# Optimization experiments

Measured on AMD Instinct MI355X. Metric: run time of the kernel, lower is better.

The kernel has to match this reference:

```python
import jax, jax.numpy as jnp
import numpy as np
import math

B, P = 4096, 512
WDT = 10          # lyr_wdt = number of irreps (multiplicity)
EPS2 = 1e-12      # NormActivation epsilon=1e-6, squared


def setup_inputs() -> dict:
    key = jax.random.key(0)
    ks = jax.random.split(key, 8)
    return {
        "invar_2b": jax.random.normal(ks[0], (B, P, 5), jnp.float32),
        "vectors_2b": jax.random.normal(ks[1], (B, P, 9), jnp.float32),
        # torch.nn.Linear params (stored as [in, out])
        "w1_0": jax.random.normal(ks[2], (5, WDT), jnp.float32) / math.sqrt(5.0),
        "b1_0": jnp.zeros((WDT,), jnp.float32),
        "w1_1": jax.random.normal(ks[3], (WDT, WDT), jnp.float32) / math.sqrt(float(WDT)),
        "b1_1": jnp.zeros((WDT,), jnp.float32),
        # o3.Linear weights (N(0,1) init, e3nn normalizes by sqrt(mul_in) in forward)
        "lin0_w": jax.random.normal(ks[4], (3, WDT), jnp.float32),
        "na0_b": jnp.zeros((WDT,), jnp.float32),   # NormActivation bias
        "lin1_w": jax.random.normal(ks[5], (WDT, WDT), jnp.float32),
        "na1_b": jnp.zeros((WDT,), jnp.float32),
        "final_w": jax.random.normal(ks[6], (WDT, 1), jnp.float32),
    }


def _self_intrc(x, w, bias):
    """o3.Linear (mul_in x 1o -> mul_out x 1o) + NormActivation(tanh, eps=1e-6, bias).

    x: [B, P, mul_in, 3]
    """
    mul_in = x.shape[-2]
    # single l=1 -> l=1 path; e3nn o3.Linear scales by 1/sqrt(fan_in)
    y = jnp.einsum('bpuc,uw->bpwc', x, w) / jnp.sqrt(jnp.float32(mul_in))
    # NormActivation: norm per irrep, clamped at eps^2 before sqrt
    n = jnp.sqrt(jnp.maximum(jnp.sum(y * y, axis=-1), EPS2))  # [B,P,mul_out]
    s = jnp.tanh(n + bias) / n                                # act(norm+b)/norm
    return y * s[..., None]


def reference(invar_2b, vectors_2b, w1_0, b1_0, w1_1, b1_1,
              lin0_w, na0_b, lin1_w, na1_b, final_w):
    # scalar branch: Linear(5,10) + ReLU, Linear(10,10) + ReLU
    y = jax.nn.relu(invar_2b @ w1_0 + b1_0)
    y = jax.nn.relu(y @ w1_1 + b1_1)              # [B, P, WDT] (10x0e)

    # equivariant branch: two self_intrc blocks on 3x1o -> 10x1o -> 10x1o
    v = vectors_2b.reshape(B, P, 3, 3)            # [B,P,3 irreps,3 comps]
    x = _self_intrc(v, lin0_w, na0_b)             # [B,P,WDT,3]
    x = _self_intrc(x, lin1_w, na1_b)             # [B,P,WDT,3]

    # ElementwiseTensorProduct(10x0e, 10x1o) -> 10x1o: per-irrep scalar gating
    x = y[..., None] * x                          # [B,P,WDT,3]

    # final o3.Linear 10x1o -> 1x1o
    x = jnp.einsum('bpuc,uw->bpwc', x, final_w) / jnp.sqrt(jnp.float32(WDT))
    return jnp.sum(x[..., 0, :], axis=1)          # sum over pairs -> [B, 3]
```

## Files before the change

### kernel.cpp

```cpp
#include <hip/hip_runtime.h>
#include <math.h>

#define BB 4096
#define PP 512
#define WDT 10
#define NP 4
#define NT 128

typedef float float2v __attribute__((ext_vector_type(2)));
typedef float float4v __attribute__((ext_vector_type(4)));

#define PKFMA(a, b, c) __builtin_elementwise_fma(a, b, c)
#define PKMAX(a, b)    __builtin_elementwise_max(a, b)
#define FENCE()        __builtin_amdgcn_sched_barrier(0)

__device__ __forceinline__ float2v bc2(float s) { return (float2v){s, s}; }

__device__ __forceinline__ float fast_tanh(float x) {
    float e = __builtin_amdgcn_exp2f(x * 2.8853900817779268f);
    return 1.0f - 2.0f * __builtin_amdgcn_rcpf(e + 1.0f);
}

__global__ __launch_bounds__(NT) void frc_2b_kernel(
    const float* __restrict__ invar,
    const float* __restrict__ vectors,
    const float* __restrict__ w1_0,
    const float* __restrict__ b1_0,
    const float* __restrict__ w1_1,
    const float* __restrict__ b1_1,
    const float* __restrict__ lin0_w,
    const float* __restrict__ na0_b,
    const float* __restrict__ lin1_w,
    const float* __restrict__ na1_b,
    const float* __restrict__ final_w,
    float* __restrict__ out)
{
    __shared__ float red[2][3];

    const int b   = blockIdx.x;
    const int tid = threadIdx.x;

    const float* iv0 = invar   + ((size_t)b * PP + tid * NP) * 5;
    const float* vv0 = vectors + ((size_t)b * PP + tid * NP) * 9;
    float in5a[NP][5];
    float v[NP][9];
    #pragma unroll
    for (int q = 0; q < 5; ++q) {
        float4v f = ((const float4v*)iv0)[q];
        #pragma unroll
        for (int r = 0; r < 4; ++r) {
            int idx = q * 4 + r;
            in5a[idx / 5][idx % 5] = f[r];
        }
    }
    #pragma unroll
    for (int q = 0; q < 9; ++q) {
        float4v f = ((const float4v*)vv0)[q];
        #pragma unroll
        for (int r = 0; r < 4; ++r) {
            int idx = q * 4 + r;
            v[idx / 9][idx % 9] = f[r];
        }
    }

    const float k3sq  = 0.33333333333333333f;
    const float k3k10 = 0.18257418583505536f;
    const float k10   = 0.31622776601683794f;
    const float2v z2  = {0.f, 0.f};

    float2v yp[NP][5];
    #pragma unroll
    for (int jp = 0; jp < 5; ++jp) {
        float2v bb = *(const float2v*)(b1_0 + 2 * jp);
        #pragma unroll
        for (int pr = 0; pr < NP; ++pr) yp[pr][jp] = bb;
    }
    #pragma unroll
    for (int i = 0; i < 5; ++i) {
        #pragma unroll
        for (int jp = 0; jp < 5; ++jp) {
            float2v wp = *(const float2v*)(w1_0 + i * WDT + 2 * jp);
            #pragma unroll
            for (int pr = 0; pr < NP; ++pr)
                yp[pr][jp] = PKFMA(wp, bc2(in5a[pr][i]), yp[pr][jp]);
        }
    }
    #pragma unroll
    for (int pr = 0; pr < NP; ++pr)
        #pragma unroll
        for (int jp = 0; jp < 5; ++jp) yp[pr][jp] = PKMAX(yp[pr][jp], z2);
    FENCE();

    float2v y2p[NP][5];
    #pragma unroll
    for (int jp = 0; jp < 5; ++jp) {
        float2v bb = *(const float2v*)(b1_1 + 2 * jp);
        #pragma unroll
        for (int pr = 0; pr < NP; ++pr) y2p[pr][jp] = bb;
    }
    #pragma unroll
    for (int k = 0; k < 5; ++k) {
        #pragma unroll
        for (int jp = 0; jp < 5; ++jp) {
            float2v wp = *(const float2v*)(w1_1 + k * WDT + 2 * jp);
            #pragma unroll
            for (int pr = 0; pr < NP; ++pr)
                y2p[pr][jp] = PKFMA(wp, bc2(yp[pr][k >> 1][k & 1]), y2p[pr][jp]);
        }
    }
    FENCE();
    #pragma unroll
    for (int k = 5; k < WDT; ++k) {
        #pragma unroll
        for (int jp = 0; jp < 5; ++jp) {
            float2v wp = *(const float2v*)(w1_1 + k * WDT + 2 * jp);
            #pragma unroll
            for (int pr = 0; pr < NP; ++pr)
                y2p[pr][jp] = PKFMA(wp, bc2(yp[pr][k >> 1][k & 1]), y2p[pr][jp]);
        }
    }
    #pragma unroll
    for (int pr = 0; pr < NP; ++pr)
        #pragma unroll
        for (int jp = 0; jp < 5; ++jp) y2p[pr][jp] = PKMAX(y2p[pr][jp], z2);
    FENCE();

    float2v c0p[NP][5], c1p[NP][5], c2p[NP][5];
    #pragma unroll
    for (int pr = 0; pr < NP; ++pr)
        #pragma unroll
        for (int jp = 0; jp < 5; ++jp) { c0p[pr][jp] = z2; c1p[pr][jp] = z2; c2p[pr][jp] = z2; }
    #pragma unroll
    for (int u = 0; u < 3; ++u) {
        #pragma unroll
        for (int jp = 0; jp < 5; ++jp) {
            float2v wp = *(const float2v*)(lin0_w + u * WDT + 2 * jp);
            #pragma unroll
            for (int pr = 0; pr < NP; ++pr) {
                c0p[pr][jp] = PKFMA(wp, bc2(v[pr][u * 3 + 0]), c0p[pr][jp]);
                c1p[pr][jp] = PKFMA(wp, bc2(v[pr][u * 3 + 1]), c1p[pr][jp]);
                c2p[pr][jp] = PKFMA(wp, bc2(v[pr][u * 3 + 2]), c2p[pr][jp]);
            }
        }
    }
    float2v x0p[NP][5], x1p[NP][5], x2p[NP][5];
    #pragma unroll
    for (int jp = 0; jp < 5; ++jp) {
        float2v nab = *(const float2v*)(na0_b + 2 * jp);
        #pragma unroll
        for (int pr = 0; pr < NP; ++pr) {
            float2v n2p = PKFMA(c0p[pr][jp], c0p[pr][jp],
                          PKFMA(c1p[pr][jp], c1p[pr][jp], c2p[pr][jp] * c2p[pr][jp]));
            float2v mp  = PKMAX(n2p * bc2(k3sq), bc2(1e-12f));
            float fh[2];
            #pragma unroll
            for (int h = 0; h < 2; ++h) {
                float m     = mp[h];
                float inv_n = __builtin_amdgcn_rsqf(m);
                float n     = m * inv_n;
                float t     = fast_tanh(n + nab[h]);
                fh[h] = t * inv_n * k3k10;
            }
            float2v fp = {fh[0], fh[1]};
            x0p[pr][jp] = c0p[pr][jp] * fp;
            x1p[pr][jp] = c1p[pr][jp] * fp;
            x2p[pr][jp] = c2p[pr][jp] * fp;
        }
    }
    FENCE();

    float2v e0p[NP][5], e1p[NP][5], e2p[NP][5];
    #pragma unroll
    for (int pr = 0; pr < NP; ++pr)
        #pragma unroll
        for (int jp = 0; jp < 5; ++jp) { e0p[pr][jp] = z2; e1p[pr][jp] = z2; e2p[pr][jp] = z2; }
    #pragma unroll
    for (int u = 0; u < 5; ++u) {
        #pragma unroll
        for (int jp = 0; jp < 5; ++jp) {
            float2v wp = *(const float2v*)(lin1_w + u * WDT + 2 * jp);
            #pragma unroll
            for (int pr = 0; pr < NP; ++pr) {
                e0p[pr][jp] = PKFMA(wp, bc2(x0p[pr][u >> 1][u & 1]), e0p[pr][jp]);
                e1p[pr][jp] = PKFMA(wp, bc2(x1p[pr][u >> 1][u & 1]), e1p[pr][jp]);
                e2p[pr][jp] = PKFMA(wp, bc2(x2p[pr][u >> 1][u & 1]), e2p[pr][jp]);
            }
        }
    }
    FENCE();
    #pragma unroll
    for (int u = 5; u < WDT; ++u) {
        #pragma unroll
        for (int jp = 0; jp < 5; ++jp) {
            float2v wp = *(const float2v*)(lin1_w + u * WDT + 2 * jp);
            #pragma unroll
            for (int pr = 0; pr < NP; ++pr) {
                e0p[pr][jp] = PKFMA(wp, bc2(x0p[pr][u >> 1][u & 1]), e0p[pr][jp]);
                e1p[pr][jp] = PKFMA(wp, bc2(x1p[pr][u >> 1][u & 1]), e1p[pr][jp]);
                e2p[pr][jp] = PKFMA(wp, bc2(x2p[pr][u >> 1][u & 1]), e2p[pr][jp]);
            }
        }
    }
    FENCE();

    float2v a0p = z2, a1p = z2, a2p = z2;
    #pragma unroll
    for (int jp = 0; jp < 5; ++jp) {
        float2v nab = *(const float2v*)(na1_b + 2 * jp);
        float2v fwp = *(const float2v*)(final_w + 2 * jp);
        #pragma unroll
        for (int pr = 0; pr < NP; ++pr) {
            float2v n2p = PKFMA(e0p[pr][jp], e0p[pr][jp],
                          PKFMA(e1p[pr][jp], e1p[pr][jp], e2p[pr][jp] * e2p[pr][jp]));
            float2v mp  = PKMAX(n2p, bc2(1e-12f));
            float gh[2];
            #pragma unroll
            for (int h = 0; h < 2; ++h) {
                float m     = mp[h];
                float inv_n = __builtin_amdgcn_rsqf(m);
                float n     = m * inv_n;
                float t     = fast_tanh(n + nab[h]);
                gh[h] = y2p[pr][jp][h] * t * inv_n * fwp[h];
            }
            float2v gp = {gh[0], gh[1]};
            a0p = PKFMA(e0p[pr][jp], gp, a0p);
            a1p = PKFMA(e1p[pr][jp], gp, a1p);
            a2p = PKFMA(e2p[pr][jp], gp, a2p);
        }
    }
    float acc0 = (a0p[0] + a0p[1]) * k10;
    float acc1 = (a1p[0] + a1p[1]) * k10;
    float acc2 = (a2p[0] + a2p[1]) * k10;

    #pragma unroll
    for (int off = 32; off > 0; off >>= 1) {
        acc0 += __shfl_down(acc0, off, 64);
        acc1 += __shfl_down(acc1, off, 64);
        acc2 += __shfl_down(acc2, off, 64);
    }
    const int wave = tid >> 6;
    if ((tid & 63) == 0) { red[wave][0] = acc0; red[wave][1] = acc1; red[wave][2] = acc2; }
    __syncthreads();
    if (tid == 0) {
        out[b * 3 + 0] = red[0][0] + red[1][0];
        out[b * 3 + 1] = red[0][1] + red[1][1];
        out[b * 3 + 2] = red[0][2] + red[1][2];
    }
}

extern "C" void kernel_launch(void* const* d_in, const int* in_sizes, int n_in,
                              void* d_out, int out_size, void* d_ws, size_t ws_size,
                              hipStream_t stream) {
    const float* invar   = (const float*)d_in[0];
    const float* vectors = (const float*)d_in[1];
    const float* w1_0    = (const float*)d_in[2];
    const float* b1_0    = (const float*)d_in[3];
    const float* w1_1    = (const float*)d_in[4];
    const float* b1_1    = (const float*)d_in[5];
    const float* lin0_w  = (const float*)d_in[6];
    const float* na0_b   = (const float*)d_in[7];
    const float* lin1_w  = (const float*)d_in[8];
    const float* na1_b   = (const float*)d_in[9];
    const float* final_w = (const float*)d_in[10];
    float* out = (float*)d_out;

    frc_2b_kernel<<<BB, NT, 0, stream>>>(invar, vectors, w1_0, b1_0, w1_1, b1_1,
                                         lin0_w, na0_b, lin1_w, na1_b, final_w, out);
}
```

Before: 184.5 us.

## Use 512-thread blocks covering two batch rows with two pairs per thread

Each thread now handles two pairs instead of four, and each block spans two batch rows with 512 threads, so the grid is halved. Loads switch from float4 to float2 vectors, and the reduction is reworked to sum four waves per row. The aim is more threads in flight to hide memory latency and fewer blocks to launch. The cost is less per-thread ILP and float2 loads that are less wide.

```diff
diff --git a/kernel.cpp b/kernel.cpp
--- a/kernel.cpp
+++ b/kernel.cpp
@@ -4,11 +4,10 @@
 #define BB 4096
 #define PP 512
 #define WDT 10
-#define NP 4
-#define NT 128
+#define NT 512
+#define NP 2
 
 typedef float float2v __attribute__((ext_vector_type(2)));
-typedef float float4v __attribute__((ext_vector_type(4)));
 
 #define PKFMA(a, b, c) __builtin_elementwise_fma(a, b, c)
 #define PKMAX(a, b)    __builtin_elementwise_max(a, b)
@@ -35,31 +34,31 @@
     const float* __restrict__ final_w,
     float* __restrict__ out)
 {
-    __shared__ float red[2][3];
-
-    const int b   = blockIdx.x;
+    __shared__ float red[8][3];
+
     const int tid = threadIdx.x;
-
-    const float* iv0 = invar   + ((size_t)b * PP + tid * NP) * 5;
-    const float* vv0 = vectors + ((size_t)b * PP + tid * NP) * 9;
+    const size_t g = (size_t)blockIdx.x * 1024 + (size_t)tid * 2;
+
+    const float* iv = invar   + g * 5;
+    const float* vv = vectors + g * 9;
+    float2v ivl[5], vvl[9];
+    #pragma unroll
+    for (int q = 0; q < 5; ++q) ivl[q] = ((const float2v*)iv)[q];
+    #pragma unroll
+    for (int q = 0; q < 9; ++q) vvl[q] = ((const float2v*)vv)[q];
     float in5a[NP][5];
     float v[NP][9];
     #pragma unroll
-    for (int q = 0; q < 5; ++q) {
-        float4v f = ((const float4v*)iv0)[q];
-        #pragma unroll
-        for (int r = 0; r < 4; ++r) {
-            int idx = q * 4 + r;
-            in5a[idx / 5][idx % 5] = f[r];
-        }
-    }
-    #pragma unroll
-    for (int q = 0; q < 9; ++q) {
-        float4v f = ((const float4v*)vv0)[q];
-        #pragma unroll
-        for (int r = 0; r < 4; ++r) {
-            int idx = q * 4 + r;
-            v[idx / 9][idx % 9] = f[r];
+    for (int pr = 0; pr < NP; ++pr) {
+        #pragma unroll
+        for (int i = 0; i < 5; ++i) {
+            int u = pr * 5 + i;
+            in5a[pr][i] = ivl[u >> 1][u & 1];
+        }
+        #pragma unroll
+        for (int i = 0; i < 9; ++i) {
+            int u = pr * 9 + i;
+            v[pr][i] = vvl[u >> 1][u & 1];
         }
     }
 
@@ -241,10 +240,20 @@
     const int wave = tid >> 6;
     if ((tid & 63) == 0) { red[wave][0] = acc0; red[wave][1] = acc1; red[wave][2] = acc2; }
     __syncthreads();
-    if (tid == 0) {
-        out[b * 3 + 0] = red[0][0] + red[1][0];
-        out[b * 3 + 1] = red[0][1] + red[1][1];
-        out[b * 3 + 2] = red[0][2] + red[1][2];
+    if ((tid & 255) == 0) {
+        const int row  = tid >> 8;
+        const int base = row * 4;
+        float r0 = 0.f, r1 = 0.f, r2 = 0.f;
+        #pragma unroll
+        for (int wv = 0; wv < 4; ++wv) {
+            r0 += red[base + wv][0];
+            r1 += red[base + wv][1];
+            r2 += red[base + wv][2];
+        }
+        const int b = blockIdx.x * 2 + row;
+        out[b * 3 + 0] = r0;
+        out[b * 3 + 1] = r1;
+        out[b * 3 + 2] = r2;
     }
 }
 
@@ -264,6 +273,6 @@
     const float* final_w = (const float*)d_in[10];
     float* out = (float*)d_out;
 
-    frc_2b_kernel<<<BB, NT, 0, stream>>>(invar, vectors, w1_0, b1_0, w1_1, b1_1,
-                                         lin0_w, na0_b, lin1_w, na1_b, final_w, out);
+    frc_2b_kernel<<<BB / 2, NT, 0, stream>>>(invar, vectors, w1_0, b1_0, w1_1, b1_1,
+                                             lin0_w, na0_b, lin1_w, na1_b, final_w, out);
 }
```

New measurement: 183.5 us. No clear change (-0.5%).
